# Kernel optimization log

Hardware: AMD Instinct MI355X
Metric: run time of the kernel (lower is better)

## Reference

```python
import jax, jax.numpy as jnp
import numpy as np

B, S, K, N, GROUP = 4, 8, 4096, 11008, 128
NUM_GROUPS = K // GROUP  # 32


def setup_inputs() -> dict:
    key = jax.random.key(0)
    k1, k2, k3 = jax.random.split(key, 3)
    x = jax.random.normal(k1, (B, S, K), dtype=jnp.float16)
    # packed int4 weights: each byte holds two nibbles (low nibble = even k, high = odd k)
    weight_packed = jax.random.randint(k2, (N, K // 2), 0, 256, dtype=jnp.int32)
    # scales: abs(randn)*0.1 in fp16, as in the torch module
    scales = (jnp.abs(jax.random.normal(k3, (N, NUM_GROUPS), dtype=jnp.float16)) * jnp.float16(0.1))
    return {"x": x, "weight_packed": weight_packed, "scales": scales}


def _dequant(weight_packed, scales, Kd):
    # unpack: low nibble -> even index k, high nibble -> odd index k+1
    n = weight_packed.shape[0]
    low = weight_packed & 0xF
    high = (weight_packed >> 4) & 0xF
    w = jnp.stack([low, high], axis=-1).reshape(n, Kd)  # [N, K] int in [0,16)
    g = Kd // scales.shape[1]
    # group-wise dequant: scale * (w - 8), scale applied in fp32 (matches fp32-accum kernel)
    wq = (w.astype(jnp.float32) - 8.0).reshape(n, scales.shape[1], g)
    wdeq = wq * scales.astype(jnp.float32)[:, :, None]
    return wdeq.reshape(n, Kd)  # [N, K] fp32


def reference(x, weight_packed, scales):
    b, s, kd = x.shape
    wdeq = _dequant(weight_packed, scales, kd)           # [N, K]
    x2 = x.reshape(-1, kd).astype(jnp.float32)           # [M, K], fp32 accumulation
    out = jnp.einsum('mk,nk->mn', x2, wdeq)              # [M, N]
    return out.astype(jnp.float16).reshape(b, s, -1)
```

## Files before the change

kernel.cpp:

```cpp
#include <hip/hip_runtime.h>

#define M 32
#define N 11008
#define K 4096
#define NGROUPS 32
#define BN 16
#define KSPLIT 8
#define KRANGE (K / KSPLIT)
#define KWAVE (KRANGE / 4)

typedef _Float16 half8 __attribute__((ext_vector_type(8)));
typedef _Float16 half4 __attribute__((ext_vector_type(4)));
typedef float floatx4 __attribute__((ext_vector_type(4)));

__device__ inline void gll16(const void* g, void* l) {
    __builtin_amdgcn_global_load_lds(
        (const __attribute__((address_space(1))) unsigned int*)g,
        (__attribute__((address_space(3))) unsigned int*)l, 16, 0, 0);
}

__device__ inline half8 unpack8(int4 wv) {
    uint4 uw; unsigned int b;
    b = (unsigned)wv.x; uw.x = ((b | (b << 12)) & 0x000F000Fu) | 0x64006400u;
    b = (unsigned)wv.y; uw.y = ((b | (b << 12)) & 0x000F000Fu) | 0x64006400u;
    b = (unsigned)wv.z; uw.z = ((b | (b << 12)) & 0x000F000Fu) | 0x64006400u;
    b = (unsigned)wv.w; uw.w = ((b | (b << 12)) & 0x000F000Fu) | 0x64006400u;
    const half8 c1032 = (half8)(_Float16)1032.0f;
    return __builtin_bit_cast(half8, uw) - c1032;
}

__global__ __launch_bounds__(512) void xcvt_kernel(
    const float* __restrict__ x, _Float16* __restrict__ xf)
{
    int i = (blockIdx.x * 512 + threadIdx.x) * 4;
    float4 v = *(const float4*)(x + i);
    half4 h;
    h[0] = (_Float16)v.x; h[1] = (_Float16)v.y;
    h[2] = (_Float16)v.z; h[3] = (_Float16)v.w;
    *(half4*)(xf + i) = h;
}

#define WAITV(n) asm volatile("s_waitcnt vmcnt(" #n ")" ::: "memory")
#define SB() __builtin_amdgcn_sched_barrier(0)

__global__ __launch_bounds__(256) void int4_gemm_kernel(
    const _Float16* __restrict__ xf,
    const int* __restrict__ wp,
    const float* __restrict__ scales,
    float* __restrict__ out)
{
    __shared__ int wsh[4096];

    const int t    = threadIdx.x;
    const int lane = t & 63;
    const int w    = t >> 6;
    const int n0   = blockIdx.x * BN;
    const int ks   = blockIdx.y;
    const int col  = lane & 15;
    const int quad = lane >> 4;
    const int kw   = ks * KRANGE + w * KWAVE;

    const float s = scales[(long)(n0 + col) * NGROUPS + ks * 4 + w];
    SB();

    const int* gw = wp + (long)(n0 + col) * (K / 2) + (kw >> 1) + quad * 4;
    #pragma unroll
    for (int j = 0; j < 4; ++j)
        gll16(gw + j * 16, &wsh[(w * 4 + j) * 256]);
    SB();

    const _Float16* gx0 = xf + (long)col * K + kw + quad * 8;
    const _Float16* gx1 = gx0 + 16 * K;
    half8 xa[4], xb[4];
    #pragma unroll
    for (int j = 0; j < 4; ++j) {
        xa[j] = *(const half8*)(gx0 + j * 32);
        xb[j] = *(const half8*)(gx1 + j * 32);
    }
    SB();

    WAITV(8);
    SB();

    floatx4 acc0 = {0,0,0,0}, acc1 = {0,0,0,0};
    #pragma unroll
    for (int j = 0; j < 4; ++j) {
        half8 bf = unpack8(*(const int4*)&wsh[(w * 4 + j) * 256 + lane * 4]);
        acc0 = __builtin_amdgcn_mfma_f32_16x16x32_f16(xa[j], bf, acc0, 0, 0, 0);
        acc1 = __builtin_amdgcn_mfma_f32_16x16x32_f16(xb[j], bf, acc1, 0, 0, 0);
    }

    __syncthreads();
    float* red = (float*)wsh;
    #pragma unroll
    for (int r = 0; r < 4; ++r) {
        red[w * 512 + (quad * 4 + r) * 16 + col]      = s * acc0[r];
        red[w * 512 + (quad * 4 + r + 16) * 16 + col] = s * acc1[r];
    }
    __syncthreads();
    #pragma unroll
    for (int i = 0; i < 2; ++i) {
        const int o = t + 256 * i;
        const float sum = red[o] + red[512 + o] + red[1024 + o] + red[1536 + o];
        const int m = o >> 4;
        const int n = o & 15;
        atomicAdd(&out[(long)m * N + n0 + n], sum);
    }
}

extern "C" void kernel_launch(void* const* d_in, const int* in_sizes, int n_in,
                              void* d_out, int out_size, void* d_ws, size_t ws_size,
                              hipStream_t stream) {
    const float* x      = (const float*)d_in[0];
    const int* wp       = (const int*)d_in[1];
    const float* scales = (const float*)d_in[2];
    float* out          = (float*)d_out;
    _Float16* xf16      = (_Float16*)d_ws;

    (void)hipMemsetAsync(out, 0, (size_t)M * N * sizeof(float), stream);
    xcvt_kernel<<<dim3((M * K) / (512 * 4)), 512, 0, stream>>>(x, xf16);
    int4_gemm_kernel<<<dim3(N / BN, KSPLIT), 256, 0, stream>>>(xf16, wp, scales, out);
}
```

Baseline: 150.9 us.

## Halve split-K and loop over double-buffered LDS chunks per block

Split-K drops from 8 to 4, so each block now walks four 256-wide K chunks instead of doing a single shot. Weight tiles are staged into double-buffered, padded LDS with global_load_lds, and x loads are prefetched one chunk ahead. The group scale is applied per chunk into the running accumulator. The aim is to halve the atomicAdd reduction traffic and block count, and to overlap loads with MFMA work. The cost is fewer blocks to hide latency and more registers held for the prefetched x fragments.

```diff
diff --git a/kernel.cpp b/kernel.cpp
--- a/kernel.cpp
+++ b/kernel.cpp
@@ -5,9 +5,12 @@
 #define K 4096
 #define NGROUPS 32
 #define BN 16
-#define KSPLIT 8
+#define KSPLIT 4
 #define KRANGE (K / KSPLIT)
-#define KWAVE (KRANGE / 4)
+#define BK 256
+#define NCHUNK (KRANGE / BK)
+#define WPAIR 260
+#define WTILE (8 * WPAIR)
 
 typedef _Float16 half8 __attribute__((ext_vector_type(8)));
 typedef _Float16 half4 __attribute__((ext_vector_type(4)));
@@ -49,53 +52,86 @@
     const float* __restrict__ scales,
     float* __restrict__ out)
 {
-    __shared__ int wsh[4096];
+    __shared__ int wsh[2 * WTILE];
 
     const int t    = threadIdx.x;
     const int lane = t & 63;
     const int w    = t >> 6;
     const int n0   = blockIdx.x * BN;
     const int ks   = blockIdx.y;
-    const int col  = lane & 15;
+    const int row  = lane & 15;
     const int quad = lane >> 4;
-    const int kw   = ks * KRANGE + w * KWAVE;
+    const int kb   = ks * KRANGE;
 
-    const float s = scales[(long)(n0 + col) * NGROUPS + ks * 4 + w];
+    const float* sbase = scales + (long)(n0 + row) * NGROUPS + ks * 8 + (w >> 1);
+    const float4 sv0 = *(const float4*)(sbase);
+    const float4 sv1 = *(const float4*)(sbase + 4);
     SB();
 
-    const int* gw = wp + (long)(n0 + col) * (K / 2) + (kw >> 1) + quad * 4;
-    #pragma unroll
-    for (int j = 0; j < 4; ++j)
-        gll16(gw + j * 16, &wsh[(w * 4 + j) * 256]);
-    SB();
+    const int p0 = w * 2, p1 = p0 + 1;
+    const int h32 = lane >> 5;
+    const int* ga = wp + (long)(n0 + 2 * p0 + h32) * (K / 2) + (kb >> 1) + (lane & 31) * 4;
+    const int* gb = wp + (long)(n0 + 2 * p1 + h32) * (K / 2) + (kb >> 1) + (lane & 31) * 4;
 
-    const _Float16* gx0 = xf + (long)col * K + kw + quad * 8;
+    #define STAGE(c) {                                                   \
+        gll16(ga + (c) * (BK / 2), &wsh[((c) & 1) * WTILE + p0 * WPAIR]);\
+        gll16(gb + (c) * (BK / 2), &wsh[((c) & 1) * WTILE + p1 * WPAIR]);\
+        SB();                                                            \
+    }
+
+    const _Float16* gx0 = xf + (long)row * K + kb + w * 64 + quad * 8;
     const _Float16* gx1 = gx0 + 16 * K;
-    half8 xa[4], xb[4];
-    #pragma unroll
-    for (int j = 0; j < 4; ++j) {
-        xa[j] = *(const half8*)(gx0 + j * 32);
-        xb[j] = *(const half8*)(gx1 + j * 32);
+
+    half8 xa0[NCHUNK], xa1[NCHUNK], xb0[NCHUNK], xb1[NCHUNK];
+    #define XLOAD(c) {                                   \
+        xa0[c] = *(const half8*)(gx0 + (c) * BK);        \
+        xa1[c] = *(const half8*)(gx0 + (c) * BK + 32);   \
+        xb0[c] = *(const half8*)(gx1 + (c) * BK);        \
+        xb1[c] = *(const half8*)(gx1 + (c) * BK + 32);   \
+        SB();                                            \
     }
-    SB();
 
-    WAITV(8);
-    SB();
+    STAGE(0)
+    XLOAD(0)
 
     floatx4 acc0 = {0,0,0,0}, acc1 = {0,0,0,0};
+
     #pragma unroll
-    for (int j = 0; j < 4; ++j) {
-        half8 bf = unpack8(*(const int4*)&wsh[(w * 4 + j) * 256 + lane * 4]);
-        acc0 = __builtin_amdgcn_mfma_f32_16x16x32_f16(xa[j], bf, acc0, 0, 0, 0);
-        acc1 = __builtin_amdgcn_mfma_f32_16x16x32_f16(xb[j], bf, acc1, 0, 0, 0);
+    for (int c = 0; c < NCHUNK; ++c) {
+        WAITV(4);
+        __builtin_amdgcn_s_barrier();
+        SB();
+        if (c + 1 < NCHUNK) {
+            STAGE(c + 1)
+            XLOAD(c + 1)
+        }
+
+        const float sc = (c == 0) ? sv0.x : (c == 1) ? sv0.z
+                       : (c == 2) ? sv1.x : sv1.z;
+        floatx4 t0 = {0,0,0,0}, t1 = {0,0,0,0};
+        #pragma unroll
+        for (int kk = 0; kk < 2; ++kk) {
+            const int bidx = (c & 1) * WTILE + (row >> 1) * WPAIR + (row & 1) * 128
+                           + w * 32 + kk * 16 + quad * 4;
+            half8 b = unpack8(*(const int4*)&wsh[bidx]);
+            t0 = __builtin_amdgcn_mfma_f32_16x16x32_f16(kk ? xa1[c] : xa0[c], b, t0, 0, 0, 0);
+            t1 = __builtin_amdgcn_mfma_f32_16x16x32_f16(kk ? xb1[c] : xb0[c], b, t1, 0, 0, 0);
+        }
+        #pragma unroll
+        for (int r = 0; r < 4; ++r) {
+            acc0[r] += sc * t0[r];
+            acc1[r] += sc * t1[r];
+        }
     }
+    #undef STAGE
+    #undef XLOAD
 
     __syncthreads();
     float* red = (float*)wsh;
     #pragma unroll
     for (int r = 0; r < 4; ++r) {
-        red[w * 512 + (quad * 4 + r) * 16 + col]      = s * acc0[r];
-        red[w * 512 + (quad * 4 + r + 16) * 16 + col] = s * acc1[r];
+        red[w * 512 + (quad * 4 + r) * 16 + row]      = acc0[r];
+        red[w * 512 + (quad * 4 + r + 16) * 16 + row] = acc1[r];
     }
     __syncthreads();
     #pragma unroll
```

Result: no change. 148.4 us (-1.7%).
